# Optimization experiments

Hardware: AMD Instinct MI355X
Metric: run time of the kernel (lower is better)

## Reference

```python
import jax, jax.numpy as jnp
import numpy as np

NUM_E = 20000   # entities
NUM_R = 200     # relations (rel table has 2*NUM_R rows)
H = 200         # h_dim
TD = 48         # t_dim (UnionTimeEncode: two halves of 24)
HD = TD // 2
L_HIST = 32     # padded per-(batch,k) history list length
HIS_K = 3
N_HIST = 3      # len(his_list_g)
N_LAYERS = 2    # RGCN layers (config.num_layers)
E = 200000      # edges per historical graph
BATCH = 512


def setup_inputs() -> dict:
    key = jax.random.key(0)
    ks = jax.random.split(key, 32)
    nrm = lambda k, shape, s=0.05: (jax.random.normal(k, shape, jnp.float32) * s)
    inp = {}
    # graph / index inputs (int)
    inp['src'] = jax.random.randint(ks[0], (N_HIST, E), 0, NUM_E, jnp.int32)
    inp['dst'] = jax.random.randint(ks[1], (N_HIST, E), 0, NUM_E, jnp.int32)
    inp['etype'] = jax.random.randint(ks[2], (N_HIST, E), 0, 2 * NUM_R, jnp.int32)
    inp['data'] = jax.random.randint(ks[3], (BATCH, 4), 0, NUM_R, jnp.int32)  # s,r,o,t
    inp['his_idx'] = jax.random.randint(ks[4], (BATCH, HIS_K, L_HIST), 0, NUM_E, jnp.int32)
    inp['his_len'] = jax.random.randint(ks[5], (BATCH, HIS_K), 0, L_HIST + 1, jnp.int32)
    # parameters (float)
    inp['ent'] = nrm(ks[6], (NUM_E, H), 0.5)          # EntEmb.ent (normal init)
    inp['loop_weight'] = nrm(ks[7], (H, H))           # EntEmb self-loop weight
    inp['rel'] = nrm(ks[8], (2 * NUM_R, H), 0.5)
    # UnionTimeEncode params (AbsTimeEncode v=0 + CosTimeEncode)
    basis = (1.0 / 10 ** np.linspace(0.0, 9.0, HD)).astype(np.float32)
    inp['abs_freq'] = jnp.asarray(basis)
    inp['abs_phase'] = jnp.zeros((HD,), jnp.float32)
    inp['cos_freq'] = jnp.asarray(basis)
    inp['cos_phase'] = jnp.zeros((HD,), jnp.float32)
    # RGCN (RE-GCN style Union-RGCN layer: msg=(h_src+rel_e)@Wn, mean agg, self-loop)
    inp['Wn'] = nrm(ks[9], (N_LAYERS, H, H))
    inp['Ws'] = nrm(ks[10], (N_LAYERS, H, H))
    # GRUCell (PyTorch layout)
    inp['W_ih'] = nrm(ks[11], (3 * H, H + TD))
    inp['W_hh'] = nrm(ks[12], (3 * H, H))
    inp['b_ih'] = jnp.zeros((3 * H,), jnp.float32)
    inp['b_hh'] = jnp.zeros((3 * H,), jnp.float32)
    # attention fusion
    inp['Wb_w'] = nrm(ks[13], (H, 3 * H + TD))
    inp['Wb_b'] = jnp.zeros((H,), jnp.float32)
    inp['Wc_w'] = nrm(ks[14], (1, H))
    inp['Wc_b'] = jnp.zeros((1,), jnp.float32)
    # decoder (MLP query @ entity table)
    inp['Wd_w'] = nrm(ks[15], (H, 3 * H))
    inp['Wd_b'] = jnp.zeros((H,), jnp.float32)
    return inp


def _l2n(x, eps=1e-12):
    # F.normalize: x / max(||x||, eps)
    n = jnp.linalg.norm(x, axis=-1, keepdims=True)
    return x / jnp.maximum(n, eps)


def reference(src, dst, etype, data, his_idx, his_len,
              ent, loop_weight, rel, abs_freq, abs_phase, cos_freq, cos_phase,
              Wn, Ws, W_ih, W_hh, b_ih, b_hh, Wb_w, Wb_b, Wc_w, Wc_b, Wd_w, Wd_b):
    def tenc(t):  # t: [N,1] float -> [N,TD]
        a = jnp.tanh((t + 1.0) * abs_freq + abs_phase)   # AbsTimeEncode(act=tanh)
        c = jnp.cos(t * cos_freq + cos_phase)            # CosTimeEncode
        return jnp.concatenate([a, c], axis=1)

    s_i, r_i = data[:, 0], data[:, 1]
    ent_e = ent @ loop_weight                  # EntEmb self-loop (dropout=identity, eval)
    rel_n = _l2n(rel)
    prev = _l2n(ent_e)                         # g_list[0]
    tim_cnt = N_HIST
    ones_e = jnp.ones((E,), jnp.float32)
    for i in range(N_HIST):                    # python loop over fixed #graphs
        si, di, ei = src[i], dst[i], etype[i]
        deg = jax.ops.segment_sum(ones_e, di, num_segments=NUM_E)         # in-degree
        inv = 1.0 / jnp.maximum(deg, 1.0)
        # g.update_all(copy_src, mean): zero in-degree nodes -> 0
        agg = jax.ops.segment_sum(prev[si], di, num_segments=NUM_E) * inv[:, None]
        h = _l2n(jnp.where(deg[:, None] > 0, agg, 0.0))
        tim_cnt -= 1
        tim = jnp.where(deg > 0, float(tim_cnt), 100.0)[:, None]
        te = tenc(tim)                                                     # [NUM_E,TD]
        for l in range(N_LAYERS):              # RGCN
            msg = (h[si] + rel_n[ei]) @ Wn[l]                              # [E,H]
            nagg = jax.ops.segment_sum(msg, di, num_segments=NUM_E) * inv[:, None]
            h = jax.nn.relu(nagg + h @ Ws[l])
        h = _l2n(h)
        # GRUCell(cat([h, te]), prev)
        gi = jnp.concatenate([h, te], axis=1) @ W_ih.T + b_ih
        gh = prev @ W_hh.T + b_hh
        ir, iz, iN = jnp.split(gi, 3, axis=1)
        hr, hz, hN = jnp.split(gh, 3, axis=1)
        rg = jax.nn.sigmoid(ir + hr)
        zg = jax.nn.sigmoid(iz + hz)
        ng = jnp.tanh(iN + rg * hN)
        prev = _l2n((1.0 - zg) * ng + zg * prev)
    out = prev

    q_s, q_r = out[s_i], rel_n[r_i]
    tim_cnt = min(N_HIST, HIS_K)
    s_embs, atts = [], []
    pos = jnp.arange(L_HIST)[None, :]
    for k in range(min(N_HIST, HIS_K)):
        tim_cnt -= 1
        ln = his_len[:, k]
        mask = (pos < ln[:, None]).astype(jnp.float32)                     # [B,L]
        # sparse one-hot mm + divide by length
        tmp = jnp.einsum('blh,bl->bh', out[his_idx[:, k, :]], mask)
        tmp = _l2n(tmp / jnp.maximum(ln, 1).astype(jnp.float32)[:, None])
        tim = jnp.where(ln > 0, float(tim_cnt), 100.0)[:, None]
        te = tenc(tim)                                                     # [B,TD]
        s_embs.append(tmp)
        a = jax.nn.relu(jnp.concatenate([q_s, q_r, tmp, te], 1) @ Wb_w.T + Wb_b)
        atts.append(a @ Wc_w.T + Wc_b)                                     # [B,1]
    att = jax.nn.softmax(jnp.stack(atts, axis=1), axis=1)                  # [B,K,1]
    out2 = jnp.sum(jnp.stack(s_embs, axis=1) * att, axis=1)                # bmm fusion
    # decoder: MLP query scored against all entity states
    q = jax.nn.relu(jnp.concatenate([q_s, q_r, out2], 1) @ Wd_w.T + Wd_b)
    return q @ out.T                                                       # [B,NUM_E]
```

## Files before the change

### kernel.cpp

```cpp
#include <hip/hip_runtime.h>
#include <hip/hip_bf16.h>

#define NUM_E   20000
#define H_DIM   200
#define TD_DIM  48
#define HD_DIM  24
#define L_HIST  32
#define N_HIST  3
#define E_EDGES 200000
#define BATCH   512


__device__ inline float wave_sum64(float x) {
    #pragma unroll
    for (int m = 1; m < 64; m <<= 1) x += __shfl_xor(x, m);
    return x;
}

__device__ inline ushort f2bf(float f) {
    unsigned u = __float_as_uint(f);
    u += 0x7fffu + ((u >> 16) & 1u);
    return (ushort)(u >> 16);
}
__device__ inline float bf2f(ushort u) {
    return __uint_as_float(((unsigned)u) << 16);
}
__device__ inline float4 bf4_to_f4(ushort4 v) {
    return (float4){bf2f(v.x), bf2f(v.y), bf2f(v.z), bf2f(v.w)};
}

__global__ void fill_i32(int* __restrict__ p, long n, int v) {
    long i = (long)blockIdx.x * blockDim.x + threadIdx.x;
    if (i < n) p[i] = v;
}

__global__ void bias_sum(float* __restrict__ bsum, const float* __restrict__ b_ih,
                         const float* __restrict__ b_hh) {
    int j = blockIdx.x * 256 + threadIdx.x;
    if (j < 600) bsum[j] = b_ih[j] + b_hh[j];
}

__global__ void cvt_bf16_k(ushort* __restrict__ o, const float* __restrict__ in, long n) {
    long i = (long)blockIdx.x * 256 + threadIdx.x;
    if (i < n) o[i] = f2bf(in[i]);
}

__global__ void make_lo(ushort* __restrict__ lo, const float* __restrict__ x,
                        const ushort* __restrict__ hi, long n) {
    long i = (long)blockIdx.x * 256 + threadIdx.x;
    if (i < n) lo[i] = f2bf(x[i] - bf2f(hi[i]));
}

__global__ void tcvt_bf16_k(ushort* __restrict__ o, const float* __restrict__ in, int R, int C) {
    int i = blockIdx.x * 256 + threadIdx.x;
    if (i >= R * C) return;
    int r = i / C, c = i - r * C;
    o[(size_t)c * R + r] = f2bf(in[i]);
}

struct Segs {
    const float* A[4];
    const float* B[4];
    int lda[4], ldb[4], Ks[4];
    int nseg, Ktot;
};

__device__ inline void seg_find(const Segs& sg, int gk, int& s, int& loc) {
    s = 0; loc = gk;
    #pragma unroll
    for (int t = 0; t < 3; t++) {
        if (s + 1 < sg.nseg && loc >= sg.Ks[s]) { loc -= sg.Ks[s]; s++; }
    }
}

__global__ __launch_bounds__(256) void sgemm_splitk(
    float* __restrict__ P, const Segs sg, int M, int N, int nbx, int nby,
    int KS, int tpc)
{
    __shared__ float As[32][68];
    __shared__ float Bs[32][68];

    int tot = nbx * nby;
    int tot_all = tot * KS;
    int chunk = (tot_all + 7) >> 3;
    int v = (int)(blockIdx.x & 7) * chunk + (int)(blockIdx.x >> 3);
    if (v >= tot_all) return;
    int kc = v / tot;
    int tile = v - kc * tot;
    int by = tile / nbx, bx = tile - by * nbx;
    const int bn = bx * 64;
    const int bm = by * 64;
    const int tid = threadIdx.x;
    const int m0 = (tid >> 4) * 4;
    const int n0 = (tid & 15) * 4;

    float acc[4][4];
    #pragma unroll
    for (int i = 0; i < 4; i++)
        #pragma unroll
        for (int j = 0; j < 4; j++) acc[i][j] = 0.f;

    const int Ktot = sg.Ktot;
    const int ntile = (Ktot + 31) / 32;
    const int kt0 = kc * tpc;
    const int kt1 = min(ntile, kt0 + tpc);

    const int a_m  = tid & 31;
    const int a_k4 = (tid >> 5) * 4;
    const int b1_n = tid & 63;
    const int b1_k = (tid >> 6) * 4;

    float4 ra[2], rb[2];
    auto loadA = [&](int k0) {
        int gk = k0 + a_k4;
        bool kin = gk < Ktot;
        int s = 0, loc = 0;
        if (kin) seg_find(sg, gk, s, loc);
        const float* Ab = sg.A[s];
        const int lda = sg.lda[s];
        #pragma unroll
        for (int r = 0; r < 2; r++) {
            int row = bm + a_m + 32 * r;
            float4 vv = {0.f, 0.f, 0.f, 0.f};
            if (kin && row < M) vv = *(const float4*)(Ab + (size_t)row * lda + loc);
            ra[r] = vv;
        }
    };
    auto loadB = [&](int k0) {
        #pragma unroll
        for (int r = 0; r < 2; r++) {
            int k4 = b1_k + 16 * r;
            int gk = k0 + k4;
            bool kin = gk < Ktot;
            int s = 0, loc = 0;
            if (kin) seg_find(sg, gk, s, loc);
            const float* Bb = sg.B[s];
            const int ldb = sg.ldb[s];
            int gn = bn + b1_n;
            float4 vv = {0.f, 0.f, 0.f, 0.f};
            if (kin && gn < N) vv = *(const float4*)(Bb + (size_t)gn * ldb + loc);
            rb[r] = vv;
        }
    };

    if (kt0 < kt1) {
        loadA(kt0 * 32); loadB(kt0 * 32);
        for (int t = kt0; t < kt1; t++) {
            #pragma unroll
            for (int r = 0; r < 2; r++) {
                int m = a_m + 32 * r;
                As[a_k4 + 0][m] = ra[r].x;
                As[a_k4 + 1][m] = ra[r].y;
                As[a_k4 + 2][m] = ra[r].z;
                As[a_k4 + 3][m] = ra[r].w;
            }
            #pragma unroll
            for (int r = 0; r < 2; r++) {
                int k4 = b1_k + 16 * r;
                Bs[k4 + 0][b1_n] = rb[r].x;
                Bs[k4 + 1][b1_n] = rb[r].y;
                Bs[k4 + 2][b1_n] = rb[r].z;
                Bs[k4 + 3][b1_n] = rb[r].w;
            }
            __syncthreads();
            if (t + 1 < kt1) { loadA((t + 1) * 32); loadB((t + 1) * 32); }
            #pragma unroll 8
            for (int kk = 0; kk < 32; kk++) {
                float4 b = *(float4*)&Bs[kk][n0];
                float4 av = *(float4*)&As[kk][m0];
                float a[4] = {av.x, av.y, av.z, av.w};
                #pragma unroll
                for (int i = 0; i < 4; i++) {
                    acc[i][0] += a[i] * b.x;
                    acc[i][1] += a[i] * b.y;
                    acc[i][2] += a[i] * b.z;
                    acc[i][3] += a[i] * b.w;
                }
            }
            __syncthreads();
        }
    }

    int col = bn + n0;
    if (col < N) {
        #pragma unroll
        for (int i = 0; i < 4; i++) {
            int row = bm + m0 + i;
            if (row < M) {
                float4 o = {acc[i][0], acc[i][1], acc[i][2], acc[i][3]};
                *(float4*)(P + ((size_t)kc * M + row) * N + col) = o;
            }
        }
    }
}

__global__ void reduce_relu(float* __restrict__ out, const float* __restrict__ P,
                            const float* __restrict__ bias, int MN, int N, int KS)
{
    int i = blockIdx.x * 256 + threadIdx.x;
    if (i >= MN) return;
    float s = bias[i % N];
    for (int k = 0; k < KS; k++) s += P[(size_t)k * MN + i];
    out[i] = fmaxf(s, 0.f);
}

__global__ void reduce_relu_split(ushort* __restrict__ qhi, ushort* __restrict__ qlo,
                                  const float* __restrict__ P, const float* __restrict__ bias,
                                  int MN, int N, int KS)
{
    int i = blockIdx.x * 256 + threadIdx.x;
    if (i >= MN) return;
    float s = bias[i % N];
    for (int k = 0; k < KS; k++) s += P[(size_t)k * MN + i];
    s = fmaxf(s, 0.f);
    ushort h = f2bf(s);
    qhi[i] = h;
    qlo[i] = f2bf(s - bf2f(h));
}

typedef __attribute__((ext_vector_type(8))) short bfrag;
typedef __attribute__((ext_vector_type(4))) float ffrag;

struct BfSegs {
    const ushort* A[3];
    const ushort* B[3];
    int lda[3], ldb[3], Ks[3];
    int nseg, Ktot;
};

__device__ inline void bseg_find(const BfSegs& sg, int gk, int& s, int& loc) {
    s = 0; loc = gk;
    #pragma unroll
    for (int t = 0; t < 2; t++) {
        if (s + 1 < sg.nseg && loc >= sg.Ks[s]) { loc -= sg.Ks[s]; s++; }
    }
}

struct GemmDesc {
    BfSegs sg;
    float* C;
    ushort* Cb;
    const float* bias;
    int M, N, ldc;
    int act, flags, order;
    int nbx, nby, blk0, nblk;
};

struct MultiArgs {
    GemmDesc d[3];
    int nd;
    int tot;
};

template<int DI>
__device__ __forceinline__ void gemm_body(const MultiArgs& ma, int v,
                                          ushort* __restrict__ Als,
                                          ushort* __restrict__ Bls)
{
    const GemmDesc& D = ma.d[DI];
    const BfSegs& sg = D.sg;
    const int tile = v - D.blk0;
    int by, bx;
    if (D.order == 0) { by = tile / D.nbx; bx = tile - by * D.nbx; }
    else              { bx = tile / D.nby; by = tile - bx * D.nby; }
    const int bm = by * 128, bn = bx * 64;
    const int M = D.M, N = D.N;

    const int tid  = threadIdx.x;
    const int lane = tid & 63;
    const int w    = tid >> 6;
    const int wm   = (w & 1) * 4;
    const int wn   = (w >> 1) * 2;

    ffrag acc[4][2];
    #pragma unroll
    for (int i = 0; i < 4; i++)
        #pragma unroll
        for (int j = 0; j < 2; j++) acc[i][j] = (ffrag){0.f, 0.f, 0.f, 0.f};

    const int Ktot = sg.Ktot;
    const int nkt = (Ktot + 63) >> 6;

    int a_m[4], a_kq[4], a_wc[4];
    #pragma unroll
    for (int i = 0; i < 4; i++) {
        int c = i * 256 + tid;
        a_m[i] = c & 127; a_kq[i] = c >> 7;
        a_wc[i] = ((a_m[i] >> 4) * 2 + (a_kq[i] >> 2)) * 64 + (a_kq[i] & 3) * 16 + (a_m[i] & 15);
    }
    int b_n[2], b_kq[2], b_wc[2];
    #pragma unroll
    for (int i = 0; i < 2; i++) {
        int c = i * 256 + tid;
        b_n[i] = c & 63; b_kq[i] = c >> 6;
        b_wc[i] = ((b_n[i] >> 4) * 2 + (b_kq[i] >> 2)) * 64 + (b_kq[i] & 3) * 16 + (b_n[i] & 15);
    }

    uint4 ra[4], rb[2];
    auto loadA = [&](int k0) {
        #pragma unroll
        for (int i = 0; i < 4; i++) {
            int gk = k0 + a_kq[i] * 8;
            int row = bm + a_m[i];
            uint4 vv = {0u, 0u, 0u, 0u};
            if (gk < Ktot && row < M) {
                int s, loc; bseg_find(sg, gk, s, loc);
                vv = *(const uint4*)(sg.A[s] + (size_t)row * sg.lda[s] + loc);
            }
            ra[i] = vv;
        }
    };
    auto loadB = [&](int k0) {
        #pragma unroll
        for (int i = 0; i < 2; i++) {
            int gk = k0 + b_kq[i] * 8;
            int gn = bn + b_n[i];
            uint4 vv = {0u, 0u, 0u, 0u};
            if (gk < Ktot && gn < N) {
                int s, loc; bseg_find(sg, gk, s, loc);
                vv = *(const uint4*)(sg.B[s] + (size_t)gn * sg.ldb[s] + loc);
            }
            rb[i] = vv;
        }
    };

    loadA(0); loadB(0);

    for (int t = 0; t < nkt; t++) {
        #pragma unroll
        for (int i = 0; i < 4; i++) *(uint4*)(&Als[a_wc[i] * 8]) = ra[i];
        #pragma unroll
        for (int i = 0; i < 2; i++) *(uint4*)(&Bls[b_wc[i] * 8]) = rb[i];
        __syncthreads();

        if (t + 1 < nkt) { loadA((t + 1) << 6); loadB((t + 1) << 6); }

        #pragma unroll
        for (int kt = 0; kt < 2; kt++) {
            bfrag af[4], bf[2];
            #pragma unroll
            for (int i = 0; i < 4; i++)
                af[i] = *(const bfrag*)(&Als[(((wm + i) * 2 + kt) * 64 + lane) * 8]);
            #pragma unroll
            for (int j = 0; j < 2; j++)
                bf[j] = *(const bfrag*)(&Bls[(((wn + j) * 2 + kt) * 64 + lane) * 8]);
            #pragma unroll
            for (int i = 0; i < 4; i++)
                #pragma unroll
                for (int j = 0; j < 2; j++)
                    acc[i][j] = __builtin_amdgcn_mfma_f32_16x16x32_bf16(af[i], bf[j], acc[i][j], 0, 0, 0);
        }
        __syncthreads();
    }

    const int rbase = (lane >> 4) * 4;
    const int cl = lane & 15;
    #pragma unroll
    for (int j = 0; j < 2; j++) {
        int col = bn + (wn + j) * 16 + cl;
        if (col >= N) continue;
        float bv = D.bias ? D.bias[col] : 0.f;
        #pragma unroll
        for (int i = 0; i < 4; i++) {
            int mrow = bm + (wm + i) * 16 + rbase;
            #pragma unroll
            for (int r = 0; r < 4; r++) {
                int row = mrow + r;
                if (row < M) {
                    float o = acc[i][j][r] + bv;
                    if (D.act == 1) o = fmaxf(o, 0.f);
                    else if (D.act == 2) o = 1.f / (1.f + expf(-o));
                    if (D.flags & 1) D.C[(size_t)row * D.ldc + col] = o;
                    if (D.flags & 2) D.Cb[(size_t)row * D.ldc + col] = f2bf(o);
                }
            }
        }
    }
}

__global__ __launch_bounds__(256) void mfma_multi(MultiArgs ma)
{
    __shared__ __align__(16) ushort Als[8192];
    __shared__ __align__(16) ushort Bls[4096];

    int tot = ma.tot;
    int chunk = (tot + 7) >> 3;
    int v = (int)(blockIdx.x & 7) * chunk + (int)(blockIdx.x >> 3);
    if (v >= tot) return;

    int di = 0;
    if (ma.nd > 1 && v >= ma.d[1].blk0) di = 1;
    if (ma.nd > 2 && v >= ma.d[2].blk0) di = 2;

    if (di == 0)      gemm_body<0>(ma, v, Als, Bls);
    else if (di == 1) gemm_body<1>(ma, v, Als, Bls);
    else              gemm_body<2>(ma, v, Als, Bls);
}


__global__ void count_dst(const int* __restrict__ di, int* __restrict__ cnt, int E) {
    int e = blockIdx.x * 256 + threadIdx.x;
    if (e < E) atomicAdd(&cnt[di[e]], 1);
}

__global__ __launch_bounds__(1024) void scan_rows(
    const int* __restrict__ cnt, int* __restrict__ row_start, int* __restrict__ cursor,
    float* __restrict__ degf, float* __restrict__ invd)
{
    __shared__ int part[1024];
    const int CH = (NUM_E + 1023) / 1024;
    int t = threadIdx.x;
    int base = t * CH;
    int local[32];
    int s = 0;
    for (int j = 0; j < CH; j++) {
        int idx = base + j;
        int c = (idx < NUM_E) ? cnt[idx] : 0;
        local[j] = s; s += c;
    }
    part[t] = s;
    __syncthreads();
    for (int off = 1; off < 1024; off <<= 1) {
        int vv = (t >= off) ? part[t - off] : 0;
        __syncthreads();
        part[t] += vv;
        __syncthreads();
    }
    int pre = (t == 0) ? 0 : part[t - 1];
    for (int j = 0; j < CH; j++) {
        int idx = base + j;
        if (idx < NUM_E) {
            int rs = pre + local[j];
            row_start[idx] = rs;
            cursor[idx] = rs;
            int c = cnt[idx];
            degf[idx] = (float)c;
            invd[idx] = 1.f / fmaxf((float)c, 1.f);
        }
    }
    if (t == 1023) row_start[NUM_E] = part[1023];
}

__global__ void build_perm(const int* __restrict__ si, const int* __restrict__ di,
                           const int* __restrict__ ei, int* __restrict__ cursor,
                           int* __restrict__ ssrc, int* __restrict__ setype, int E)
{
    int e = blockIdx.x * 256 + threadIdx.x;
    if (e >= E) return;
    int pos = atomicAdd(&cursor[di[e]], 1);
    ssrc[pos]   = si[e];
    setype[pos] = ei[e];
}


__global__ __launch_bounds__(256) void seg_gather_norm_bf(
    ushort* __restrict__ bh, const ushort* __restrict__ bprev,
    const int* __restrict__ ssrc, const int* __restrict__ row_start,
    const float* __restrict__ invd)
{
    int v = blockIdx.x * 4 + (threadIdx.x >> 6);
    int lane = threadIdx.x & 63;
    if (v >= NUM_E) return;
    int s0 = row_start[v], s1 = row_start[v + 1];
    bool act = lane < 50;
    float4 acc = {0.f, 0.f, 0.f, 0.f};
    int j = s0;
    for (; j + 1 < s1; j += 2) {
        int sa = ssrc[j], sb = ssrc[j + 1];
        if (act) {
            float4 xa = bf4_to_f4(*(const ushort4*)(bprev + (long)sa * H_DIM + lane * 4));
            float4 xb = bf4_to_f4(*(const ushort4*)(bprev + (long)sb * H_DIM + lane * 4));
            acc.x += xa.x + xb.x; acc.y += xa.y + xb.y;
            acc.z += xa.z + xb.z; acc.w += xa.w + xb.w;
        }
    }
    if (j < s1) {
        int sa = ssrc[j];
        if (act) {
            float4 xa = bf4_to_f4(*(const ushort4*)(bprev + (long)sa * H_DIM + lane * 4));
            acc.x += xa.x; acc.y += xa.y; acc.z += xa.z; acc.w += xa.w;
        }
    }
    float iv = invd[v];
    acc.x *= iv; acc.y *= iv; acc.z *= iv; acc.w *= iv;
    float ss = act ? (acc.x*acc.x + acc.y*acc.y + acc.z*acc.z + acc.w*acc.w) : 0.f;
    ss = wave_sum64(ss);
    float r = 1.f / fmaxf(sqrtf(ss), 1e-12f);
    if (act) {
        ushort4 ob = {f2bf(acc.x * r), f2bf(acc.y * r), f2bf(acc.z * r), f2bf(acc.w * r)};
        *(ushort4*)(bh + (long)v * H_DIM + lane * 4) = ob;
    }
}

__global__ __launch_bounds__(256) void seg_gather_layer_bf(
    ushort* __restrict__ btmp, const ushort* __restrict__ bh, const ushort* __restrict__ brel,
    const int* __restrict__ ssrc, const int* __restrict__ setype,
    const int* __restrict__ row_start, const float* __restrict__ invd)
{
    int v = blockIdx.x * 4 + (threadIdx.x >> 6);
    int lane = threadIdx.x & 63;
    if (v >= NUM_E) return;
    int s0 = row_start[v], s1 = row_start[v + 1];
    bool act = lane < 50;
    float4 acc = {0.f, 0.f, 0.f, 0.f};
    int j = s0;
    for (; j + 1 < s1; j += 2) {
        int sa = ssrc[j], ta = setype[j];
        int sb = ssrc[j + 1], tb = setype[j + 1];
        if (act) {
            float4 xa = bf4_to_f4(*(const ushort4*)(bh   + (long)sa * H_DIM + lane * 4));
            float4 ya = bf4_to_f4(*(const ushort4*)(brel + (long)ta * H_DIM + lane * 4));
            float4 xb = bf4_to_f4(*(const ushort4*)(bh   + (long)sb * H_DIM + lane * 4));
            float4 yb = bf4_to_f4(*(const ushort4*)(brel + (long)tb * H_DIM + lane * 4));
            acc.x += (xa.x + ya.x) + (xb.x + yb.x);
            acc.y += (xa.y + ya.y) + (xb.y + yb.y);
            acc.z += (xa.z + ya.z) + (xb.z + yb.z);
            acc.w += (xa.w + ya.w) + (xb.w + yb.w);
        }
    }
    if (j < s1) {
        int s = ssrc[j];
        int t = setype[j];
        if (act) {
            float4 x = bf4_to_f4(*(const ushort4*)(bh   + (long)s * H_DIM + lane * 4));
            float4 y = bf4_to_f4(*(const ushort4*)(brel + (long)t * H_DIM + lane * 4));
            acc.x += x.x + y.x; acc.y += x.y + y.y;
            acc.z += x.z + y.z; acc.w += x.w + y.w;
        }
    }
    float iv = invd[v];
    if (act) {
        ushort4 ob = {f2bf(acc.x * iv), f2bf(acc.y * iv), f2bf(acc.z * iv), f2bf(acc.w * iv)};
        *(ushort4*)(btmp + (long)v * H_DIM + lane * 4) = ob;
    }
}


__global__ __launch_bounds__(256) void l2norm_rows4(
    float* __restrict__ out, ushort* __restrict__ bout,
    const float* __restrict__ in, int nrows)
{
    int v = blockIdx.x * 4 + (threadIdx.x >> 6);
    int lane = threadIdx.x & 63;
    if (v >= nrows) return;
    bool act = lane < 50;
    float4 x = {0.f, 0.f, 0.f, 0.f};
    if (act) x = *(const float4*)(in + (long)v * H_DIM + lane * 4);
    float ss = x.x*x.x + x.y*x.y + x.z*x.z + x.w*x.w;
    ss = wave_sum64(ss);
    float r = 1.f / fmaxf(sqrtf(ss), 1e-12f);
    if (act) {
        long base = (long)v * H_DIM + lane * 4;
        float4 o = {x.x * r, x.y * r, x.z * r, x.w * r};
        *(float4*)(out + base) = o;
        if (bout) {
            ushort4 ob = {f2bf(o.x), f2bf(o.y), f2bf(o.z), f2bf(o.w)};
            *(ushort4*)(bout + base) = ob;
        }
    }
}

__global__ __launch_bounds__(256) void l2norm_bf4(ushort* __restrict__ b, int nrows)
{
    int v = blockIdx.x * 4 + (threadIdx.x >> 6);
    int lane = threadIdx.x & 63;
    if (v >= nrows) return;
    bool act = lane < 50;
    float4 x = {0.f, 0.f, 0.f, 0.f};
    long base = (long)v * H_DIM + lane * 4;
    if (act) x = bf4_to_f4(*(const ushort4*)(b + base));
    float ss = x.x*x.x + x.y*x.y + x.z*x.z + x.w*x.w;
    ss = wave_sum64(ss);
    float r = 1.f / fmaxf(sqrtf(ss), 1e-12f);
    if (act) {
        ushort4 ob = {f2bf(x.x * r), f2bf(x.y * r), f2bf(x.z * r), f2bf(x.w * r)};
        *(ushort4*)(b + base) = ob;
    }
}

__global__ void tenc_table(ushort* __restrict__ tbl, const float* __restrict__ af,
                           const float* __restrict__ ap, const float* __restrict__ cf,
                           const float* __restrict__ cp, float tcnt)
{
    int j = threadIdx.x;
    if (j >= 128) return;
    int half = j >> 6;
    int jj = j & 63;
    if (jj >= TD_DIM) return;
    float t = half ? 100.0f : tcnt;
    float val;
    if (jj < HD_DIM) val = tanhf((t + 1.f) * af[jj] + ap[jj]);
    else             val = cosf(t * cf[jj - HD_DIM] + cp[jj - HD_DIM]);
    tbl[half * 64 + jj] = f2bf(val);
}

__global__ void tenc_fill(ushort* __restrict__ bte, const float* __restrict__ deg,
                          const ushort* __restrict__ tbl, int M)
{
    int idx = blockIdx.x * 256 + threadIdx.x;
    if (idx >= M * 6) return;
    int v = idx / 6, c = idx - v * 6;
    int base = (deg[v] > 0.f) ? 0 : 64;
    *(uint4*)(bte + (long)v * TD_DIM + c * 8) = *(const uint4*)(tbl + base + c * 8);
}

__global__ __launch_bounds__(256) void gru_fused(
    float* __restrict__ prev, ushort* __restrict__ bprev, const float* __restrict__ rz,
    const float* __restrict__ iN, const float* __restrict__ hN)
{
    int v = blockIdx.x * 4 + (threadIdx.x >> 6);
    int lane = threadIdx.x & 63;
    if (v >= NUM_E) return;
    bool act = lane < 50;
    long b200 = (long)v * H_DIM + lane * 4;
    long b400 = (long)v * 400 + lane * 4;
    float4 o = {0.f, 0.f, 0.f, 0.f};
    if (act) {
        float4 r4 = *(const float4*)(rz + b400);
        float4 z4 = *(const float4*)(rz + b400 + 200);
        float4 n4 = *(const float4*)(iN + b200);
        float4 g4 = *(const float4*)(hN + b200);
        float4 p4 = *(const float4*)(prev + b200);
        float ngx = tanhf(n4.x + r4.x * g4.x);
        float ngy = tanhf(n4.y + r4.y * g4.y);
        float ngz = tanhf(n4.z + r4.z * g4.z);
        float ngw = tanhf(n4.w + r4.w * g4.w);
        o.x = (1.f - z4.x) * ngx + z4.x * p4.x;
        o.y = (1.f - z4.y) * ngy + z4.y * p4.y;
        o.z = (1.f - z4.z) * ngz + z4.z * p4.z;
        o.w = (1.f - z4.w) * ngw + z4.w * p4.w;
    }
    float ss = o.x*o.x + o.y*o.y + o.z*o.z + o.w*o.w;
    ss = wave_sum64(ss);
    float r = 1.f / fmaxf(sqrtf(ss), 1e-12f);
    if (act) {
        float4 wv = {o.x * r, o.y * r, o.z * r, o.w * r};
        *(float4*)(prev + b200) = wv;
        ushort4 ob = {f2bf(wv.x), f2bf(wv.y), f2bf(wv.z), f2bf(wv.w)};
        *(ushort4*)(bprev + b200) = ob;
    }
}


__global__ void gather_qs_qr3(float* __restrict__ qs3, float* __restrict__ qr3,
                              const float* __restrict__ out, const float* __restrict__ reln,
                              const int* __restrict__ data)
{
    long i = (long)blockIdx.x * 256 + threadIdx.x;
    if (i >= (long)BATCH * H_DIM) return;
    int b = (int)(i / H_DIM), j = (int)(i % H_DIM);
    float vs = out[(long)data[b * 4 + 0] * H_DIM + j];
    float vr = reln[(long)data[b * 4 + 1] * H_DIM + j];
    const long S = (long)BATCH * H_DIM;
    qs3[i] = vs; qs3[i + S] = vs; qs3[i + 2*S] = vs;
    qr3[i] = vr; qr3[i + S] = vr; qr3[i + 2*S] = vr;
}

__global__ __launch_bounds__(64) void semb_kernel(
    float* __restrict__ semb, const float* __restrict__ out,
    const int* __restrict__ his_idx, const int* __restrict__ his_len)
{
    int b = blockIdx.x, k = blockIdx.y;
    int lane = threadIdx.x;
    int ln = his_len[b * 3 + k];
    if (ln > L_HIST) ln = L_HIST;
    float vals[4] = {0.f, 0.f, 0.f, 0.f};
    for (int l = 0; l < ln; l++) {
        int idx = his_idx[((long)b * 3 + k) * L_HIST + l];
        #pragma unroll
        for (int t = 0; t < 4; t++) {
            int j = lane + t * 64;
            if (j < H_DIM) vals[t] += out[(long)idx * H_DIM + j];
        }
    }
    float scale = 1.f / fmaxf((float)ln, 1.f);
    float ss = 0.f;
    #pragma unroll
    for (int t = 0; t < 4; t++) { vals[t] *= scale; ss += vals[t] * vals[t]; }
    ss = wave_sum64(ss);
    float r = 1.f / fmaxf(sqrtf(ss), 1e-12f);
    #pragma unroll
    for (int t = 0; t < 4; t++) {
        int j = lane + t * 64;
        if (j < H_DIM) semb[((long)k * BATCH + b) * H_DIM + j] = vals[t] * r;
    }
}

__global__ void tenc_batch(float* __restrict__ teb, const int* __restrict__ his_len,
                           const float* __restrict__ af, const float* __restrict__ ap,
                           const float* __restrict__ cf, const float* __restrict__ cp)
{
    int idx = blockIdx.x * 256 + threadIdx.x;
    if (idx >= 3 * BATCH * TD_DIM) return;
    int k = idx / (BATCH * TD_DIM);
    int rem = idx - k * (BATCH * TD_DIM);
    int b = rem / TD_DIM, j = rem % TD_DIM;
    int ln = his_len[b * 3 + k];
    float t = (ln > 0) ? (float)(2 - k) : 100.0f;
    float val;
    if (j < HD_DIM) val = tanhf((t + 1.f) * af[j] + ap[j]);
    else            val = cosf(t * cf[j - HD_DIM] + cp[j - HD_DIM]);
    teb[idx] = val;
}

__global__ __launch_bounds__(256) void att_logits_rows(
    float* __restrict__ atts, const float* __restrict__ a,
    const float* __restrict__ Wc_w, const float* __restrict__ Wc_b)
{
    int row = blockIdx.x * 4 + (threadIdx.x >> 6);
    int lane = threadIdx.x & 63;
    if (row >= 3 * BATCH) return;
    int k = row >> 9;
    int b = row & 511;
    float s = 0.f;
    for (int j = lane; j < H_DIM; j += 64) s += a[(long)row * H_DIM + j] * Wc_w[j];
    s = wave_sum64(s);
    if (lane == 0) atts[b * 3 + k] = s + Wc_b[0];
}

__global__ void softmax_out2(float* __restrict__ out2, const float* __restrict__ atts,
                             const float* __restrict__ semb)
{
    long i = (long)blockIdx.x * 256 + threadIdx.x;
    if (i >= (long)BATCH * H_DIM) return;
    int b = (int)(i / H_DIM), j = (int)(i % H_DIM);
    float l0 = atts[b * 3 + 0], l1 = atts[b * 3 + 1], l2 = atts[b * 3 + 2];
    float m = fmaxf(l0, fmaxf(l1, l2));
    float e0 = expf(l0 - m), e1 = expf(l1 - m), e2 = expf(l2 - m);
    float s = e0 + e1 + e2;
    float v = (e0 * semb[((long)0 * BATCH + b) * H_DIM + j] +
               e1 * semb[((long)1 * BATCH + b) * H_DIM + j] +
               e2 * semb[((long)2 * BATCH + b) * H_DIM + j]) / s;
    out2[i] = v;
}


extern "C" void kernel_launch(void* const* d_in, const int* in_sizes, int n_in,
                              void* d_out, int out_size, void* d_ws, size_t ws_size,
                              hipStream_t stream)
{
    (void)in_sizes; (void)n_in; (void)out_size; (void)ws_size;

    const int*   src     = (const int*)d_in[0];
    const int*   dst     = (const int*)d_in[1];
    const int*   etype   = (const int*)d_in[2];
    const int*   data    = (const int*)d_in[3];
    const int*   his_idx = (const int*)d_in[4];
    const int*   his_len = (const int*)d_in[5];
    const float* ent     = (const float*)d_in[6];
    const float* loop_w  = (const float*)d_in[7];
    const float* rel     = (const float*)d_in[8];
    const float* af      = (const float*)d_in[9];
    const float* ap      = (const float*)d_in[10];
    const float* cf      = (const float*)d_in[11];
    const float* cp      = (const float*)d_in[12];
    const float* Wn      = (const float*)d_in[13];
    const float* Ws      = (const float*)d_in[14];
    const float* W_ih    = (const float*)d_in[15];
    const float* W_hh    = (const float*)d_in[16];
    const float* b_ih    = (const float*)d_in[17];
    const float* b_hh    = (const float*)d_in[18];
    const float* Wb_w    = (const float*)d_in[19];
    const float* Wb_b    = (const float*)d_in[20];
    const float* Wc_w    = (const float*)d_in[21];
    const float* Wc_b    = (const float*)d_in[22];
    const float* Wd_w    = (const float*)d_in[23];
    const float* Wd_b    = (const float*)d_in[24];
    float* out_p = (float*)d_out;

    float* wp = (float*)d_ws;
    size_t off = 0;
    auto alloc = [&](size_t n) {
        size_t n4 = (n + 3) & ~(size_t)3;
        float* p = wp + off; off += n4; return p;
    };
    const long nE200 = (long)NUM_E * H_DIM;
    float* prev   = alloc(nE200);
    float* h1     = alloc(nE200);
    float* tmp    = alloc(nE200);
    float* rz     = out_p;
    ushort* bh0   = (ushort*)alloc(nE200 / 2);
    ushort* bh1   = (ushort*)alloc(nE200 / 2);
    ushort* btmp  = (ushort*)alloc(nE200 / 2);
    ushort* bprev = (ushort*)alloc(nE200 / 2);
    ushort* plo   = (ushort*)alloc(nE200 / 2);
    ushort* bte   = (ushort*)alloc((size_t)NUM_E * TD_DIM / 2);
    ushort* brel  = (ushort*)alloc(400 * H_DIM / 2);
    ushort* bW_ih = (ushort*)alloc(600 * 248 / 2);
    ushort* bW_hh = (ushort*)alloc(600 * 200 / 2);
    ushort* bWn_t = (ushort*)alloc(2 * 200 * 200 / 2);
    ushort* bWs_t = (ushort*)alloc(2 * 200 * 200 / 2);
    ushort* bLp_t = (ushort*)alloc(200 * 200 / 2);
    ushort* qhi   = (ushort*)alloc(BATCH * H_DIM / 2);
    ushort* qlo   = (ushort*)alloc(BATCH * H_DIM / 2);
    ushort* ttbl  = (ushort*)alloc(64);
    float* degf   = alloc(NUM_E);
    float* invd   = alloc(NUM_E);
    float* reln   = alloc(400 * H_DIM);
    float* bsum   = alloc(1024);
    float* qs3    = alloc(3 * BATCH * H_DIM);
    float* qr3    = alloc(3 * BATCH * H_DIM);
    float* semb   = alloc(3 * BATCH * H_DIM);
    float* teb    = alloc(3 * BATCH * TD_DIM);
    float* abuf   = alloc(3 * BATCH * H_DIM);
    float* atts   = alloc(2048);
    float* out2   = alloc(BATCH * H_DIM);
    int* cnt       = (int*)alloc(NUM_E);
    int* row_start = (int*)alloc(NUM_E + 4);
    int* cursor    = (int*)alloc(NUM_E);
    int* ssrc      = (int*)alloc(E_EDGES);
    int* setype    = (int*)alloc(E_EDGES);

    auto nblk = [](long n) { return (unsigned)((n + 255) / 256); };

    auto bseg1 = [](const ushort* A, int la, const ushort* B, int lb, int K) {
        BfSegs s{}; s.A[0]=A; s.lda[0]=la; s.B[0]=B; s.ldb[0]=lb; s.Ks[0]=K;
        s.nseg=1; s.Ktot=K; return s;
    };
    auto bseg2 = [](const ushort* A0, int la0, const ushort* B0, int lb0, int K0,
                    const ushort* A1, int la1, const ushort* B1, int lb1, int K1) {
        BfSegs s{}; s.A[0]=A0; s.lda[0]=la0; s.B[0]=B0; s.ldb[0]=lb0; s.Ks[0]=K0;
        s.A[1]=A1; s.lda[1]=la1; s.B[1]=B1; s.ldb[1]=lb1; s.Ks[1]=K1;
        s.nseg=2; s.Ktot=K0+K1; return s;
    };
    auto bseg3 = [](const ushort* A0, int la0, const ushort* B0, int lb0, int K0,
                    const ushort* A1, int la1, const ushort* B1, int lb1, int K1,
                    const ushort* A2, int la2, const ushort* B2, int lb2, int K2) {
        BfSegs s{}; s.A[0]=A0; s.lda[0]=la0; s.B[0]=B0; s.ldb[0]=lb0; s.Ks[0]=K0;
        s.A[1]=A1; s.lda[1]=la1; s.B[1]=B1; s.ldb[1]=lb1; s.Ks[1]=K1;
        s.A[2]=A2; s.lda[2]=la2; s.B[2]=B2; s.ldb[2]=lb2; s.Ks[2]=K2;
        s.nseg=3; s.Ktot=K0+K1+K2; return s;
    };

    auto desc = [](const BfSegs& sg, float* C, ushort* Cb, const float* bias,
                   int M, int N, int ldc, int act, int flags, int order) {
        GemmDesc D{}; D.sg=sg; D.C=C; D.Cb=Cb; D.bias=bias;
        D.M=M; D.N=N; D.ldc=ldc; D.act=act; D.flags=flags; D.order=order;
        D.nbx=(N+63)>>6; D.nby=(M+127)>>7; D.nblk=D.nbx*D.nby; D.blk0=0;
        return D;
    };
    auto launch_multi = [&](GemmDesc* ds, int nd) {
        MultiArgs ma{};
        int tot = 0;
        for (int i = 0; i < nd; i++) { ds[i].blk0 = tot; tot += ds[i].nblk; ma.d[i] = ds[i]; }
        ma.nd = nd; ma.tot = tot;
        unsigned grid = (unsigned)(((tot + 7) >> 3) << 3);
        mfma_multi<<<grid, 256, 0, stream>>>(ma);
    };

    auto seg3 = [](const float* A0, int la0, const float* B0, int lb0, int K0,
                   const float* A1, int la1, const float* B1, int lb1, int K1,
                   const float* A2, int la2, const float* B2, int lb2, int K2) {
        Segs s{}; s.A[0]=A0; s.lda[0]=la0; s.B[0]=B0; s.ldb[0]=lb0; s.Ks[0]=K0;
        s.A[1]=A1; s.lda[1]=la1; s.B[1]=B1; s.ldb[1]=lb1; s.Ks[1]=K1;
        s.A[2]=A2; s.lda[2]=la2; s.B[2]=B2; s.ldb[2]=lb2; s.Ks[2]=K2;
        s.nseg=3; s.Ktot=K0+K1+K2; return s;
    };
    auto seg4 = [](const float* A0, int la0, const float* B0, int lb0, int K0,
                   const float* A1, int la1, const float* B1, int lb1, int K1,
                   const float* A2, int la2, const float* B2, int lb2, int K2,
                   const float* A3, int la3, const float* B3, int lb3, int K3) {
        Segs s{}; s.A[0]=A0; s.lda[0]=la0; s.B[0]=B0; s.ldb[0]=lb0; s.Ks[0]=K0;
        s.A[1]=A1; s.lda[1]=la1; s.B[1]=B1; s.ldb[1]=lb1; s.Ks[1]=K1;
        s.A[2]=A2; s.lda[2]=la2; s.B[2]=B2; s.ldb[2]=lb2; s.Ks[2]=K2;
        s.A[3]=A3; s.lda[3]=la3; s.B[3]=B3; s.ldb[3]=lb3; s.Ks[3]=K3;
        s.nseg=4; s.Ktot=K0+K1+K2+K3; return s;
    };
    auto splitk = [&](float* P, const Segs& sg, int M, int N, int KS) {
        int nbx = (N + 63) >> 6;
        int nby = (M + 63) >> 6;
        int ntile = (sg.Ktot + 31) / 32;
        int tpc = (ntile + KS - 1) / KS;
        int tot_all = nbx * nby * KS;
        unsigned grid = (unsigned)(((tot_all + 7) >> 3) << 3);
        sgemm_splitk<<<grid, 256, 0, stream>>>(P, sg, M, N, nbx, nby, KS, tpc);
    };

    const unsigned r4 = (NUM_E + 3) / 4;

    l2norm_rows4<<<100, 256, 0, stream>>>(reln, brel, rel, 400);
    bias_sum<<<3, 256, 0, stream>>>(bsum, b_ih, b_hh);
    cvt_bf16_k<<<nblk(600L*248), 256, 0, stream>>>(bW_ih, W_ih, 600L*248);
    cvt_bf16_k<<<nblk(600L*200), 256, 0, stream>>>(bW_hh, W_hh, 600L*200);
    tcvt_bf16_k<<<nblk(40000), 256, 0, stream>>>(bLp_t, loop_w, 200, 200);
    tcvt_bf16_k<<<nblk(40000), 256, 0, stream>>>(bWn_t,          Wn,          200, 200);
    tcvt_bf16_k<<<nblk(40000), 256, 0, stream>>>(bWn_t + 40000,  Wn + 40000,  200, 200);
    tcvt_bf16_k<<<nblk(40000), 256, 0, stream>>>(bWs_t,          Ws,          200, 200);
    tcvt_bf16_k<<<nblk(40000), 256, 0, stream>>>(bWs_t + 40000,  Ws + 40000,  200, 200);

    cvt_bf16_k<<<nblk(nE200), 256, 0, stream>>>(btmp, ent, nE200);
    {
        GemmDesc d0 = desc(bseg1(btmp, H_DIM, bLp_t, H_DIM, H_DIM),
                           tmp, nullptr, nullptr, NUM_E, H_DIM, H_DIM, 0, 1, 0);
        launch_multi(&d0, 1);
    }
    l2norm_rows4<<<r4, 256, 0, stream>>>(prev, bprev, tmp, NUM_E);

    for (int i = 0; i < N_HIST; i++) {
        const int* si = src   + (long)i * E_EDGES;
        const int* di = dst   + (long)i * E_EDGES;
        const int* ei = etype + (long)i * E_EDGES;
        float tcnt = (float)(N_HIST - 1 - i);

        fill_i32<<<nblk(NUM_E), 256, 0, stream>>>(cnt, NUM_E, 0);
        count_dst<<<nblk(E_EDGES), 256, 0, stream>>>(di, cnt, E_EDGES);
        scan_rows<<<1, 1024, 0, stream>>>(cnt, row_start, cursor, degf, invd);
        build_perm<<<nblk(E_EDGES), 256, 0, stream>>>(si, di, ei, cursor, ssrc, setype, E_EDGES);

        seg_gather_norm_bf<<<r4, 256, 0, stream>>>(bh0, bprev, ssrc, row_start, invd);
        tenc_table<<<1, 128, 0, stream>>>(ttbl, af, ap, cf, cp, tcnt);
        tenc_fill<<<nblk((long)NUM_E * 6), 256, 0, stream>>>(bte, degf, ttbl, NUM_E);

        seg_gather_layer_bf<<<r4, 256, 0, stream>>>(btmp, bh0, brel, ssrc, setype, row_start, invd);
        {
            GemmDesc d0 = desc(bseg2(btmp, H_DIM, bWn_t,         H_DIM, H_DIM,
                                     bh0,  H_DIM, bWs_t,         H_DIM, H_DIM),
                               nullptr, bh1, nullptr, NUM_E, H_DIM, H_DIM, 1, 2, 0);
            launch_multi(&d0, 1);
        }
        seg_gather_layer_bf<<<r4, 256, 0, stream>>>(btmp, bh1, brel, ssrc, setype, row_start, invd);
        {
            GemmDesc d0 = desc(bseg2(btmp, H_DIM, bWn_t + 40000, H_DIM, H_DIM,
                                     bh1,  H_DIM, bWs_t + 40000, H_DIM, H_DIM),
                               nullptr, bh0, nullptr, NUM_E, H_DIM, H_DIM, 1, 2, 0);
            launch_multi(&d0, 1);
        }
        l2norm_bf4<<<r4, 256, 0, stream>>>(bh0, NUM_E);

        {
            GemmDesc d3[3];
            d3[0] = desc(bseg3(bh0,   H_DIM,  bW_ih,       248, H_DIM,
                               bte,   TD_DIM, bW_ih + 200, 248, TD_DIM,
                               bprev, H_DIM,  bW_hh,       200, H_DIM),
                         rz, nullptr, bsum, NUM_E, 400, 400, 2, 1, 0);
            d3[1] = desc(bseg2(bh0, H_DIM,  bW_ih + 400*248,       248, H_DIM,
                               bte, TD_DIM, bW_ih + 400*248 + 200, 248, TD_DIM),
                         h1, nullptr, b_ih + 400, NUM_E, H_DIM, H_DIM, 0, 1, 0);
            d3[2] = desc(bseg1(bprev, H_DIM, bW_hh + 400*200, 200, H_DIM),
                         tmp, nullptr, b_hh + 400, NUM_E, H_DIM, H_DIM, 0, 1, 0);
            launch_multi(d3, 3);
        }

        gru_fused<<<r4, 256, 0, stream>>>(prev, bprev, rz, h1, tmp);
    }

    gather_qs_qr3<<<nblk((long)BATCH * H_DIM), 256, 0, stream>>>(qs3, qr3, prev, reln, data);
    semb_kernel<<<dim3(BATCH, 3), 64, 0, stream>>>(semb, prev, his_idx, his_len);
    tenc_batch<<<nblk(3L * BATCH * TD_DIM), 256, 0, stream>>>(teb, his_len, af, ap, cf, cp);

    {
        const int KS = 8;
        const int MN = 3 * BATCH * H_DIM;
        splitk(h1, seg4(qs3, H_DIM,  Wb_w,       648, H_DIM,
                        qr3, H_DIM,  Wb_w + 200, 648, H_DIM,
                        semb, H_DIM, Wb_w + 400, 648, H_DIM,
                        teb, TD_DIM, Wb_w + 600, 648, TD_DIM),
               3 * BATCH, H_DIM, KS);
        reduce_relu<<<nblk(MN), 256, 0, stream>>>(abuf, h1, Wb_b, MN, H_DIM, KS);
    }
    att_logits_rows<<<(3 * BATCH + 3) / 4, 256, 0, stream>>>(atts, abuf, Wc_w, Wc_b);
    softmax_out2<<<nblk((long)BATCH * H_DIM), 256, 0, stream>>>(out2, atts, semb);

    {
        const int KS = 8;
        const int MN = BATCH * H_DIM;
        splitk(tmp, seg3(qs3, H_DIM,  Wd_w,       600, H_DIM,
                         qr3, H_DIM,  Wd_w + 200, 600, H_DIM,
                         out2, H_DIM, Wd_w + 400, 600, H_DIM),
               BATCH, H_DIM, KS);
        reduce_relu_split<<<nblk(MN), 256, 0, stream>>>(qhi, qlo, tmp, Wd_b, MN, H_DIM, KS);
    }

    make_lo<<<nblk(nE200), 256, 0, stream>>>(plo, prev, bprev, nE200);

    {
        GemmDesc d0 = desc(bseg3(qhi, H_DIM, bprev, H_DIM, H_DIM,
                                 qhi, H_DIM, plo,   H_DIM, H_DIM,
                                 qlo, H_DIM, bprev, H_DIM, H_DIM),
                           out_p, nullptr, nullptr, BATCH, NUM_E, NUM_E, 0, 1, 1);
        launch_multi(&d0, 1);
    }
}
```

Baseline: 1.343 ms.

## Replace LDS-tiled MFMA GEMM with register-streaming per-wave GEMM specialized on K

The shared-memory 128x64 block-tiled GEMM is replaced by a kernel in which each wave owns a 16-column strip. The wave holds the whole K extent of B in registers and streams four 16-row A sub-tiles straight from global memory into MFMA, with no LDS or barriers. K-tile count and segment count become template parameters so loops fully unroll for each GEMM shape. This removes LDS staging and synchronization for these small-K (200-648) GEMMs. In exchange A is re-read from global or cache by every column wave, with less reuse, and register pressure is high, up to 19 uint4 of B per lane.

Measured after the change: 1.823 ms. +35.8%, slower.

```diff
diff --git a/kernel.cpp b/kernel.cpp
--- a/kernel.cpp
+++ b/kernel.cpp
@@ -228,173 +228,122 @@
     int nseg, Ktot;
 };
 
-__device__ inline void bseg_find(const BfSegs& sg, int gk, int& s, int& loc) {
+struct SDesc {
+    const ushort* A[3];
+    const ushort* B[3];
+    int lda[3], ldb[3], Ks[3];
+    int Ktot, M, N, ldc;
+    int ncw, nwv, woff;
+    int act, flags, tag;
+    const float* bias;
+    float* C;
+    ushort* Cb;
+};
+
+struct SArgs { SDesc d[3]; int nd; int totw; };
+
+template<int NSEG>
+__device__ __forceinline__ void sfind(const SDesc& D, int gk, int& s, int& loc) {
     s = 0; loc = gk;
     #pragma unroll
-    for (int t = 0; t < 2; t++) {
-        if (s + 1 < sg.nseg && loc >= sg.Ks[s]) { loc -= sg.Ks[s]; s++; }
-    }
-}
-
-struct GemmDesc {
-    BfSegs sg;
-    float* C;
-    ushort* Cb;
-    const float* bias;
-    int M, N, ldc;
-    int act, flags, order;
-    int nbx, nby, blk0, nblk;
-};
-
-struct MultiArgs {
-    GemmDesc d[3];
-    int nd;
-    int tot;
-};
-
-template<int DI>
-__device__ __forceinline__ void gemm_body(const MultiArgs& ma, int v,
-                                          ushort* __restrict__ Als,
-                                          ushort* __restrict__ Bls)
-{
-    const GemmDesc& D = ma.d[DI];
-    const BfSegs& sg = D.sg;
-    const int tile = v - D.blk0;
-    int by, bx;
-    if (D.order == 0) { by = tile / D.nbx; bx = tile - by * D.nbx; }
-    else              { bx = tile / D.nby; by = tile - bx * D.nby; }
-    const int bm = by * 128, bn = bx * 64;
-    const int M = D.M, N = D.N;
-
-    const int tid  = threadIdx.x;
-    const int lane = tid & 63;
-    const int w    = tid >> 6;
-    const int wm   = (w & 1) * 4;
-    const int wn   = (w >> 1) * 2;
-
-    ffrag acc[4][2];
+    for (int t = 0; t < NSEG - 1; t++) {
+        if (loc >= D.Ks[s]) { loc -= D.Ks[s]; s++; }
+    }
+}
+
+template<int NKT, int NSEG>
+__device__ __forceinline__ void stream_body(const SDesc& D, int wv)
+{
+    const int ncw = D.ncw;
+    const int mc = wv / ncw;
+    const int cw = wv - mc * ncw;
+    const int m0 = mc * 64;
+    const int lane = (int)(threadIdx.x & 63);
+    const int cl = lane & 15;
+    const int kg = lane >> 4;
+    const int col = cw * 16 + cl;
+    const bool colok = col < D.N;
+    const int Ktot = D.Ktot;
+
+    uint4 bfr[NKT];
     #pragma unroll
-    for (int i = 0; i < 4; i++)
+    for (int kt = 0; kt < NKT; kt++) {
+        int gk = kt * 32 + kg * 8;
+        uint4 v = {0u, 0u, 0u, 0u};
+        if (colok && gk < Ktot) {
+            int s, loc; sfind<NSEG>(D, gk, s, loc);
+            v = *(const uint4*)(D.B[s] + (size_t)col * D.ldb[s] + loc);
+        }
+        bfr[kt] = v;
+    }
+
+    const float bv = (D.bias && colok) ? D.bias[col] : 0.f;
+
+    for (int ms = 0; ms < 4; ms++) {
+        const int row = m0 + ms * 16 + cl;
+        const bool rowok = row < D.M;
+        uint4 afr[NKT];
         #pragma unroll
-        for (int j = 0; j < 2; j++) acc[i][j] = (ffrag){0.f, 0.f, 0.f, 0.f};
-
-    const int Ktot = sg.Ktot;
-    const int nkt = (Ktot + 63) >> 6;
-
-    int a_m[4], a_kq[4], a_wc[4];
-    #pragma unroll
-    for (int i = 0; i < 4; i++) {
-        int c = i * 256 + tid;
-        a_m[i] = c & 127; a_kq[i] = c >> 7;
-        a_wc[i] = ((a_m[i] >> 4) * 2 + (a_kq[i] >> 2)) * 64 + (a_kq[i] & 3) * 16 + (a_m[i] & 15);
-    }
-    int b_n[2], b_kq[2], b_wc[2];
-    #pragma unroll
-    for (int i = 0; i < 2; i++) {
-        int c = i * 256 + tid;
-        b_n[i] = c & 63; b_kq[i] = c >> 6;
-        b_wc[i] = ((b_n[i] >> 4) * 2 + (b_kq[i] >> 2)) * 64 + (b_kq[i] & 3) * 16 + (b_n[i] & 15);
-    }
-
-    uint4 ra[4], rb[2];
-    auto loadA = [&](int k0) {
+        for (int kt = 0; kt < NKT; kt++) {
+            int gk = kt * 32 + kg * 8;
+            uint4 v = {0u, 0u, 0u, 0u};
+            if (rowok && gk < Ktot) {
+                int s, loc; sfind<NSEG>(D, gk, s, loc);
+                v = *(const uint4*)(D.A[s] + (size_t)row * D.lda[s] + loc);
+            }
+            afr[kt] = v;
+        }
+        ffrag acc = (ffrag){0.f, 0.f, 0.f, 0.f};
         #pragma unroll
-        for (int i = 0; i < 4; i++) {
-            int gk = k0 + a_kq[i] * 8;
-            int row = bm + a_m[i];
-            uint4 vv = {0u, 0u, 0u, 0u};
-            if (gk < Ktot && row < M) {
-                int s, loc; bseg_find(sg, gk, s, loc);
-                vv = *(const uint4*)(sg.A[s] + (size_t)row * sg.lda[s] + loc);
-            }
-            ra[i] = vv;
-        }
-    };
-    auto loadB = [&](int k0) {
-        #pragma unroll
-        for (int i = 0; i < 2; i++) {
-            int gk = k0 + b_kq[i] * 8;
-            int gn = bn + b_n[i];
-            uint4 vv = {0u, 0u, 0u, 0u};
-            if (gk < Ktot && gn < N) {
-                int s, loc; bseg_find(sg, gk, s, loc);
-                vv = *(const uint4*)(sg.B[s] + (size_t)gn * sg.ldb[s] + loc);
-            }
-            rb[i] = vv;
-        }
-    };
-
-    loadA(0); loadB(0);
-
-    for (int t = 0; t < nkt; t++) {
-        #pragma unroll
-        for (int i = 0; i < 4; i++) *(uint4*)(&Als[a_wc[i] * 8]) = ra[i];
-        #pragma unroll
-        for (int i = 0; i < 2; i++) *(uint4*)(&Bls[b_wc[i] * 8]) = rb[i];
-        __syncthreads();
-
-        if (t + 1 < nkt) { loadA((t + 1) << 6); loadB((t + 1) << 6); }
-
-        #pragma unroll
-        for (int kt = 0; kt < 2; kt++) {
-            bfrag af[4], bf[2];
-            #pragma unroll
-            for (int i = 0; i < 4; i++)
-                af[i] = *(const bfrag*)(&Als[(((wm + i) * 2 + kt) * 64 + lane) * 8]);
-            #pragma unroll
-            for (int j = 0; j < 2; j++)
-                bf[j] = *(const bfrag*)(&Bls[(((wn + j) * 2 + kt) * 64 + lane) * 8]);
-            #pragma unroll
-            for (int i = 0; i < 4; i++)
-                #pragma unroll
-                for (int j = 0; j < 2; j++)
-                    acc[i][j] = __builtin_amdgcn_mfma_f32_16x16x32_bf16(af[i], bf[j], acc[i][j], 0, 0, 0);
-        }
-        __syncthreads();
-    }
-
-    const int rbase = (lane >> 4) * 4;
-    const int cl = lane & 15;
-    #pragma unroll
-    for (int j = 0; j < 2; j++) {
-        int col = bn + (wn + j) * 16 + cl;
-        if (col >= N) continue;
-        float bv = D.bias ? D.bias[col] : 0.f;
-        #pragma unroll
-        for (int i = 0; i < 4; i++) {
-            int mrow = bm + (wm + i) * 16 + rbase;
+        for (int kt = 0; kt < NKT; kt++) {
+            bfrag af = *(bfrag*)&afr[kt];
+            bfrag bf = *(bfrag*)&bfr[kt];
+            acc = __builtin_amdgcn_mfma_f32_16x16x32_bf16(af, bf, acc, 0, 0, 0);
+        }
+        if (colok) {
             #pragma unroll
             for (int r = 0; r < 4; r++) {
-                int row = mrow + r;
-                if (row < M) {
-                    float o = acc[i][j][r] + bv;
+                int rr = m0 + ms * 16 + kg * 4 + r;
+                if (rr < D.M) {
+                    float o = acc[r] + bv;
                     if (D.act == 1) o = fmaxf(o, 0.f);
                     else if (D.act == 2) o = 1.f / (1.f + expf(-o));
-                    if (D.flags & 1) D.C[(size_t)row * D.ldc + col] = o;
-                    if (D.flags & 2) D.Cb[(size_t)row * D.ldc + col] = f2bf(o);
+                    if (D.flags & 1) D.C[(size_t)rr * D.ldc + col] = o;
+                    if (D.flags & 2) D.Cb[(size_t)rr * D.ldc + col] = f2bf(o);
                 }
             }
         }
     }
 }
 
-__global__ __launch_bounds__(256) void mfma_multi(MultiArgs ma)
-{
-    __shared__ __align__(16) ushort Als[8192];
-    __shared__ __align__(16) ushort Bls[4096];
-
-    int tot = ma.tot;
-    int chunk = (tot + 7) >> 3;
-    int v = (int)(blockIdx.x & 7) * chunk + (int)(blockIdx.x >> 3);
-    if (v >= tot) return;
+template<int TAG>
+__device__ __forceinline__ void run_tag(const SDesc& D, int wv) {
+    if constexpr (TAG == 0) stream_body<7, 1>(D, wv);
+    else if constexpr (TAG == 1) stream_body<13, 2>(D, wv);
+    else if constexpr (TAG == 2) stream_body<14, 3>(D, wv);
+    else if constexpr (TAG == 3) stream_body<8, 2>(D, wv);
+    else if constexpr (TAG == 4) stream_body<19, 3>(D, wv);
+}
+
+template<int T0, int T1, int T2>
+__global__ __launch_bounds__(256) void mfma_stream(SArgs sa)
+{
+    int nblk = (sa.totw + 3) >> 2;
+    int chunk = (nblk + 7) >> 3;
+    int vb = (int)(blockIdx.x & 7) * chunk + (int)(blockIdx.x >> 3);
+    if (vb >= nblk) return;
+    int gw = vb * 4 + (int)(threadIdx.x >> 6);
+    if (gw >= sa.totw) return;
 
     int di = 0;
-    if (ma.nd > 1 && v >= ma.d[1].blk0) di = 1;
-    if (ma.nd > 2 && v >= ma.d[2].blk0) di = 2;
-
-    if (di == 0)      gemm_body<0>(ma, v, Als, Bls);
-    else if (di == 1) gemm_body<1>(ma, v, Als, Bls);
-    else              gemm_body<2>(ma, v, Als, Bls);
+    if (sa.nd > 1 && gw >= sa.d[1].woff) di = 1;
+    if (sa.nd > 2 && gw >= sa.d[2].woff) di = 2;
+    const SDesc& D = sa.d[di];
+    int wv = gw - D.woff;
+
+    if (di == 0) { run_tag<T0>(D, wv); return; }
+    if constexpr (T1 >= 0) { if (di == 1) { run_tag<T1>(D, wv); return; } }
+    if constexpr (T2 >= 0) { if (di == 2) { run_tag<T2>(D, wv); return; } }
 }
 
 
@@ -832,20 +781,26 @@
         s.nseg=3; s.Ktot=K0+K1+K2; return s;
     };
 
-    auto desc = [](const BfSegs& sg, float* C, ushort* Cb, const float* bias,
-                   int M, int N, int ldc, int act, int flags, int order) {
-        GemmDesc D{}; D.sg=sg; D.C=C; D.Cb=Cb; D.bias=bias;
-        D.M=M; D.N=N; D.ldc=ldc; D.act=act; D.flags=flags; D.order=order;
-        D.nbx=(N+63)>>6; D.nby=(M+127)>>7; D.nblk=D.nbx*D.nby; D.blk0=0;
+    auto sdesc = [](const BfSegs& sg, float* C, ushort* Cb, const float* bias,
+                    int M, int N, int ldc, int act, int flags, int tag) {
+        SDesc D{};
+        for (int i = 0; i < 3; i++) {
+            D.A[i]=sg.A[i]; D.B[i]=sg.B[i];
+            D.lda[i]=sg.lda[i]; D.ldb[i]=sg.ldb[i]; D.Ks[i]=sg.Ks[i];
+        }
+        D.Ktot=sg.Ktot; D.M=M; D.N=N; D.ldc=ldc;
+        D.ncw=(N+15)>>4; D.nwv=D.ncw*((M+63)>>6); D.woff=0;
+        D.act=act; D.flags=flags; D.tag=tag; D.bias=bias; D.C=C; D.Cb=Cb;
         return D;
     };
-    auto launch_multi = [&](GemmDesc* ds, int nd) {
-        MultiArgs ma{};
+    auto margs = [](SDesc* ds, int nd, unsigned& grid) {
+        SArgs sa{};
         int tot = 0;
-        for (int i = 0; i < nd; i++) { ds[i].blk0 = tot; tot += ds[i].nblk; ma.d[i] = ds[i]; }
-        ma.nd = nd; ma.tot = tot;
-        unsigned grid = (unsigned)(((tot + 7) >> 3) << 3);
-        mfma_multi<<<grid, 256, 0, stream>>>(ma);
+        for (int i = 0; i < nd; i++) { ds[i].woff = tot; tot += ds[i].nwv; sa.d[i] = ds[i]; }
+        sa.nd = nd; sa.totw = tot;
+        unsigned nb = (unsigned)((tot + 3) >> 2);
+        grid = ((nb + 7) >> 3) << 3;
+        return sa;
     };
 
     auto seg3 = [](const float* A0, int la0, const float* B0, int lb0, int K0,
@@ -890,9 +845,10 @@
 
     cvt_bf16_k<<<nblk(nE200), 256, 0, stream>>>(btmp, ent, nE200);
     {
-        GemmDesc d0 = desc(bseg1(btmp, H_DIM, bLp_t, H_DIM, H_DIM),
-                           tmp, nullptr, nullptr, NUM_E, H_DIM, H_DIM, 0, 1, 0);
-        launch_multi(&d0, 1);
+        SDesc d0 = sdesc(bseg1(btmp, H_DIM, bLp_t, H_DIM, H_DIM),
+                         tmp, nullptr, nullptr, NUM_E, H_DIM, H_DIM, 0, 1, 0);
+        unsigned grid; SArgs sa = margs(&d0, 1, grid);
+        mfma_stream<0,-1,-1><<<grid, 256, 0, stream>>>(sa);
     }
     l2norm_rows4<<<r4, 256, 0, stream>>>(prev, bprev, tmp, NUM_E);
 
@@ -913,32 +869,35 @@
 
         seg_gather_layer_bf<<<r4, 256, 0, stream>>>(btmp, bh0, brel, ssrc, setype, row_start, invd);
         {
-            GemmDesc d0 = desc(bseg2(btmp, H_DIM, bWn_t,         H_DIM, H_DIM,
-                                     bh0,  H_DIM, bWs_t,         H_DIM, H_DIM),
-                               nullptr, bh1, nullptr, NUM_E, H_DIM, H_DIM, 1, 2, 0);
-            launch_multi(&d0, 1);
+            SDesc d0 = sdesc(bseg2(btmp, H_DIM, bWn_t,         H_DIM, H_DIM,
+                                   bh0,  H_DIM, bWs_t,         H_DIM, H_DIM),
+                             nullptr, bh1, nullptr, NUM_E, H_DIM, H_DIM, 1, 2, 1);
+            unsigned grid; SArgs sa = margs(&d0, 1, grid);
+            mfma_stream<1,-1,-1><<<grid, 256, 0, stream>>>(sa);
         }
         seg_gather_layer_bf<<<r4, 256, 0, stream>>>(btmp, bh1, brel, ssrc, setype, row_start, invd);
         {
-            GemmDesc d0 = desc(bseg2(btmp, H_DIM, bWn_t + 40000, H_DIM, H_DIM,
-                                     bh1,  H_DIM, bWs_t + 40000, H_DIM, H_DIM),
-                               nullptr, bh0, nullptr, NUM_E, H_DIM, H_DIM, 1, 2, 0);
-            launch_multi(&d0, 1);
+            SDesc d0 = sdesc(bseg2(btmp, H_DIM, bWn_t + 40000, H_DIM, H_DIM,
+                                   bh1,  H_DIM, bWs_t + 40000, H_DIM, H_DIM),
+                             nullptr, bh0, nullptr, NUM_E, H_DIM, H_DIM, 1, 2, 1);
+            unsigned grid; SArgs sa = margs(&d0, 1, grid);
+            mfma_stream<1,-1,-1><<<grid, 256, 0, stream>>>(sa);
         }
         l2norm_bf4<<<r4, 256, 0, stream>>>(bh0, NUM_E);
 
         {
-            GemmDesc d3[3];
-            d3[0] = desc(bseg3(bh0,   H_DIM,  bW_ih,       248, H_DIM,
-                               bte,   TD_DIM, bW_ih + 200, 248, TD_DIM,
-                               bprev, H_DIM,  bW_hh,       200, H_DIM),
-                         rz, nullptr, bsum, NUM_E, 400, 400, 2, 1, 0);
-            d3[1] = desc(bseg2(bh0, H_DIM,  bW_ih + 400*248,       248, H_DIM,
-                               bte, TD_DIM, bW_ih + 400*248 + 200, 248, TD_DIM),
-                         h1, nullptr, b_ih + 400, NUM_E, H_DIM, H_DIM, 0, 1, 0);
-            d3[2] = desc(bseg1(bprev, H_DIM, bW_hh + 400*200, 200, H_DIM),
-                         tmp, nullptr, b_hh + 400, NUM_E, H_DIM, H_DIM, 0, 1, 0);
-            launch_multi(d3, 3);
+            SDesc d3[3];
+            d3[0] = sdesc(bseg3(bh0,   H_DIM,  bW_ih,       248, H_DIM,
+                                bte,   TD_DIM, bW_ih + 200, 248, TD_DIM,
+                                bprev, H_DIM,  bW_hh,       200, H_DIM),
+                          rz, nullptr, bsum, NUM_E, 400, 400, 2, 1, 2);
+            d3[1] = sdesc(bseg2(bh0, H_DIM,  bW_ih + 400*248,       248, H_DIM,
+                                bte, TD_DIM, bW_ih + 400*248 + 200, 248, TD_DIM),
+                          h1, nullptr, b_ih + 400, NUM_E, H_DIM, H_DIM, 0, 1, 3);
+            d3[2] = sdesc(bseg1(bprev, H_DIM, bW_hh + 400*200, 200, H_DIM),
+                          tmp, nullptr, b_hh + 400, NUM_E, H_DIM, H_DIM, 0, 1, 0);
+            unsigned grid; SArgs sa = margs(d3, 3, grid);
+            mfma_stream<2,3,0><<<grid, 256, 0, stream>>>(sa);
         }
 
         gru_fused<<<r4, 256, 0, stream>>>(prev, bprev, rz, h1, tmp);
@@ -974,10 +933,11 @@
     make_lo<<<nblk(nE200), 256, 0, stream>>>(plo, prev, bprev, nE200);
 
     {
-        GemmDesc d0 = desc(bseg3(qhi, H_DIM, bprev, H_DIM, H_DIM,
-                                 qhi, H_DIM, plo,   H_DIM, H_DIM,
-                                 qlo, H_DIM, bprev, H_DIM, H_DIM),
-                           out_p, nullptr, nullptr, BATCH, NUM_E, NUM_E, 0, 1, 1);
-        launch_multi(&d0, 1);
-    }
-}
+        SDesc d0 = sdesc(bseg3(qhi, H_DIM, bprev, H_DIM, H_DIM,
+                               qhi, H_DIM, plo,   H_DIM, H_DIM,
+                               qlo, H_DIM, bprev, H_DIM, H_DIM),
+                         out_p, nullptr, nullptr, BATCH, NUM_E, NUM_E, 0, 1, 4);
+        unsigned grid; SArgs sa = margs(&d0, 1, grid);
+        mfma_stream<4,-1,-1><<<grid, 256, 0, stream>>>(sa);
+    }
+}
```
